# Performance work log

Hardware: AMD Instinct MI355X
Metric: run time of the kernel (lower is better)

Reference implementation:

```python
import jax, jax.numpy as jnp
import numpy as np

K_GRAD = 20        # num_nbrs for gradient operator
K_NORMAL = 10      # knn for normal/basis estimation
GRAD_REG = 1e-3    # grad_reg (lambda)
KERNEL_WIDTH = 1.0 # grad_kernel_width
EPS = 1e-8
N1, N2 = 8192, 8192
CHANNELS = [3, 64, 128, 256]


def knn_idx(pos, k):
    # brute-force kNN incl. self (loop=True, target_to_source)
    sq = jnp.sum(pos * pos, axis=1)
    d2 = sq[:, None] + sq[None, :] - 2.0 * (pos @ pos.T)
    _, idx = jax.lax.top_k(-d2, k)
    return idx  # [N, k]


def estimate_basis(pos, nbr, orientation):
    rel = pos[nbr] - pos[:, None, :]              # [N,k,3]
    cov = jnp.einsum('nki,nkj->nij', rel, rel)    # [N,3,3] local PCA
    _, vecs = jnp.linalg.eigh(cov)                # ascending eigenvalues
    normal, x_basis = vecs[:, :, 0], vecs[:, :, 2]
    sign = jnp.where(jnp.sum(normal * orientation, -1, keepdims=True) < 0.0, -1.0, 1.0)
    normal = normal * sign                        # orient along `orientation`
    y_basis = jnp.cross(normal, x_basis)
    return normal, x_basis, y_basis


def build_grad_div(pos, x_basis, y_basis, nbr):
    # regularized, Gaussian-weighted least-squares fit of a linear function per neighborhood
    rel = pos[nbr] - pos[:, None, :]              # [N,k,3]
    u = jnp.einsum('nkd,nd->nk', rel, x_basis)    # tangent coords
    v = jnp.einsum('nkd,nd->nk', rel, y_basis)
    dist = jnp.sqrt(jnp.sum(rel * rel, -1) + EPS)
    h = jnp.mean(dist, axis=1, keepdims=True)     # per-point bandwidth
    w = jnp.exp(-(dist * dist) / ((KERNEL_WIDTH * h) ** 2 + EPS))
    B = jnp.stack([jnp.ones_like(u), u, v], -1)   # [N,k,3] design matrix
    BtW = jnp.swapaxes(B, 1, 2) * w[:, None, :]   # [N,3,k]
    A = BtW @ B + GRAD_REG * jnp.eye(3, dtype=pos.dtype)
    C = jnp.linalg.solve(A, BtW)                  # [N,3,k] LS coefficients
    Gx, Gy = C[:, 1, :], C[:, 2, :]               # gradient stencils
    basis = jnp.stack([x_basis, y_basis], -1)     # [N,3,2]
    R = jnp.einsum('nda,nkdb->nkab', basis, basis[nbr])  # transport j->i, [N,k,2,2]
    return Gx, Gy, R


def grad_apply(Gx, Gy, nbr, f):
    fn = f[nbr]                                   # [N,k,C]
    return jnp.stack([jnp.einsum('nk,nkc->nc', Gx, fn),
                      jnp.einsum('nk,nkc->nc', Gy, fn)], 1)  # [N,2,C]


def div_apply(Gx, Gy, R, nbr, v):
    vt = jnp.einsum('nkab,nkbc->nkac', R, v[nbr])  # transported neighbor vectors
    return (jnp.einsum('nk,nkc->nc', Gx, vt[:, :, 0]) +
            jnp.einsum('nk,nkc->nc', Gy, vt[:, :, 1]))


def delta_conv(x, v, nbr, Gx, Gy, R, Ws, bs, Wv, bv, centralized):
    xn = x[nbr]
    if centralized:
        xn = xn - x[:, None, :]
    xmax = jnp.max(xn, axis=1)                    # max aggregation
    dv = div_apply(Gx, Gy, R, nbr, v)             # divergence
    Jv = jnp.stack([-v[:, 1], v[:, 0]], 1)        # 90-degree rotation
    cv = div_apply(Gx, Gy, R, nbr, Jv)            # curl = div(J v)
    x_out = jax.nn.relu(jnp.concatenate([xmax, dv, cv], -1) @ Ws + bs)
    if Wv is None:
        return x_out, v                            # last layer: scalar only
    gv = grad_apply(Gx, Gy, nbr, x_out)           # [N,2,Cout]
    vo = jnp.concatenate([v, gv], -1) @ Wv        # channel mix, no bias (equivariant)
    n = jnp.sqrt(jnp.sum(vo * vo, axis=1, keepdims=True) + EPS)
    vo = vo * (jax.nn.relu(n + bv) / (n + EPS))   # norm-gated vector nonlinearity
    return x_out, vo


def _forward(points, als_ppoints, params):
    pos = jnp.concatenate([points, als_ppoints], axis=0)  # [N,3]
    nbr = knn_idx(pos, K_GRAD)
    nbr_n = knn_idx(pos, K_NORMAL)
    _, xb, yb = estimate_basis(pos, nbr_n, orientation=pos)
    Gx, Gy, R = build_grad_div(pos, xb, yb, nbr)
    x = pos
    v = grad_apply(Gx, Gy, nbr, x)                # v = grad @ x
    out = []
    for i, (Ws, bs, Wv, bv) in enumerate(params):
        x, v = delta_conv(x, v, nbr, Gx, Gy, R, Ws, bs, Wv, bv, centralized=(i == 0))
        out.append(x)
    return tuple(out)


def setup_inputs():
    key = jax.random.key(0)
    ks = jax.random.split(key, 8)
    inp = {
        'points': jax.random.normal(ks[0], (N1, 3), jnp.float32),
        'als_ppoints': jax.random.normal(ks[1], (N2, 3), jnp.float32),
    }
    ki = 2
    for i in range(3):
        cin, cout = CHANNELS[i], CHANNELS[i + 1]
        inp[f'Ws{i}'] = jax.random.normal(ks[ki], (3 * cin, cout), jnp.float32) / np.sqrt(3.0 * cin)
        inp[f'bs{i}'] = jnp.zeros((cout,), jnp.float32)
        ki += 1
        if i < 2:
            inp[f'Wv{i}'] = jax.random.normal(ks[ki], (cin + cout, cout), jnp.float32) / np.sqrt(float(cin + cout))
            inp[f'bv{i}'] = jnp.zeros((cout,), jnp.float32)
            ki += 1
    return inp


def reference(points, als_ppoints, Ws0, bs0, Wv0, bv0, Ws1, bs1, Wv1, bv1, Ws2, bs2):
    params = [(Ws0, bs0, Wv0, bv0), (Ws1, bs1, Wv1, bv1), (Ws2, bs2, None, None)]
    return _forward(points, als_ppoints, params)
```

## Files before the change

kernel.cpp:

```cpp
#include <hip/hip_runtime.h>
#include <math.h>

#define NPTS 16384
#define KG 20
#define KN 10
#define KC 8
#define EPSF 1e-8f

#define GDIM 32
#define GL 4.75f
#define CW 0.296875f
#define GINV 3.3684210526f
#define RMAX 6

typedef __attribute__((ext_vector_type(8))) short short8v;
typedef __attribute__((ext_vector_type(4))) float floatx4;

__device__ __forceinline__ unsigned short f2bf(float v) {
  union { float f; unsigned u; } x;
  x.f = v;
  unsigned r = x.u + 0x7FFFu + ((x.u >> 16) & 1u);
  return (unsigned short)(r >> 16);
}

__device__ __forceinline__ float bf2f(unsigned short u) {
  union { unsigned u32; float f; } x;
  x.u32 = (unsigned)u << 16;
  return x.f;
}

#define KNN_INSERT(d2v, iv)                                                 \
  if ((d2v) < dist[KG - 1]) {                                               \
    dist[KG - 1] = (d2v); idx[KG - 1] = (iv);                               \
    _Pragma("unroll")                                                       \
    for (int s_ = KG - 1; s_ > 0; --s_) {                                   \
      if (dist[s_] < dist[s_ - 1]) {                                        \
        float td_ = dist[s_]; dist[s_] = dist[s_ - 1]; dist[s_ - 1] = td_;  \
        int ti_ = idx[s_]; idx[s_] = idx[s_ - 1]; idx[s_ - 1] = ti_;        \
      }                                                                     \
    }                                                                       \
  }

#define KNN_INSERT8(d2v, iv)                                                \
  if ((d2v) < dist[KC - 1]) {                                               \
    dist[KC - 1] = (d2v); idx[KC - 1] = (iv);                               \
    _Pragma("unroll")                                                       \
    for (int s_ = KC - 1; s_ > 0; --s_) {                                   \
      if (dist[s_] < dist[s_ - 1]) {                                        \
        float td_ = dist[s_]; dist[s_] = dist[s_ - 1]; dist[s_ - 1] = td_;  \
        int ti_ = idx[s_]; idx[s_] = idx[s_ - 1]; idx[s_ - 1] = ti_;        \
      }                                                                     \
    }                                                                       \
  }

__global__ __launch_bounds__(256) void posbin_kernel(const float* __restrict__ pts,
                                                     const float* __restrict__ als,
                                                     float4* __restrict__ pos4,
                                                     int* __restrict__ cell_count,
                                                     int* __restrict__ pt_cell) {
  int n = blockIdx.x * 256 + threadIdx.x;
  if (n >= NPTS) return;
  const float* src = (n < 8192) ? (pts + (size_t)n * 3) : (als + (size_t)(n - 8192) * 3);
  float x = src[0], y = src[1], z = src[2];
  pos4[n] = make_float4(x, y, z, 0.f);
  int cxi = (int)floorf((x + GL) * GINV); cxi = min(max(cxi, 0), GDIM - 1);
  int cyi = (int)floorf((y + GL) * GINV); cyi = min(max(cyi, 0), GDIM - 1);
  int czi = (int)floorf((z + GL) * GINV); czi = min(max(czi, 0), GDIM - 1);
  int c = (czi * GDIM + cyi) * GDIM + cxi;
  pt_cell[n] = c;
  atomicAdd(&cell_count[c], 1);
}

__global__ __launch_bounds__(256) void zero_kernel(int* __restrict__ cell_count,
                                                   int* __restrict__ fb_count) {
  int i = blockIdx.x * 256 + threadIdx.x;
  if (i < GDIM * GDIM * GDIM) cell_count[i] = 0;
  if (i == 0) *fb_count = 0;
}

__device__ __forceinline__ int cell_of(float x) {
  int c = (int)floorf((x + GL) * GINV);
  return min(max(c, 0), GDIM - 1);
}

__global__ __launch_bounds__(1024) void scan_kernel(const int* __restrict__ cell_count,
                                                    int* __restrict__ cell_start,
                                                    int* __restrict__ cell_cursor) {
  __shared__ int s[1024];
  int tid = threadIdx.x;
  int base = tid * 32;
  int local[32];
  int sum = 0;
#pragma unroll
  for (int i = 0; i < 32; ++i) { local[i] = cell_count[base + i]; sum += local[i]; }
  s[tid] = sum;
  __syncthreads();
  for (int off = 1; off < 1024; off <<= 1) {
    int v = (tid >= off) ? s[tid - off] : 0;
    __syncthreads();
    s[tid] += v;
    __syncthreads();
  }
  int run = s[tid] - sum;
#pragma unroll
  for (int i = 0; i < 32; ++i) {
    cell_start[base + i] = run;
    cell_cursor[base + i] = run;
    run += local[i];
  }
}

__global__ __launch_bounds__(256) void scatter_kernel(const float4* __restrict__ pos4,
                                                      const int* __restrict__ pt_cell,
                                                      int* __restrict__ cell_cursor,
                                                      float4* __restrict__ sorted4,
                                                      int* __restrict__ sortmap) {
  int i = blockIdx.x * 256 + threadIdx.x;
  if (i >= NPTS) return;
  int c = pt_cell[i];
  int dst = atomicAdd(&cell_cursor[c], 1);
  float4 p = pos4[i];
  p.w = __int_as_float(i);
  sorted4[dst] = p;
  sortmap[dst] = i;
}

__global__ __launch_bounds__(256) void knn_grid_kernel(const float4* __restrict__ sorted4,
                                                       const int* __restrict__ cell_start,
                                                       const int* __restrict__ cell_count,
                                                       int* __restrict__ nbr,
                                                       int* __restrict__ fb_list,
                                                       int* __restrict__ fb_count) {
  int lane = threadIdx.x & 63;
  int sub = lane >> 5;
  int sl = lane & 31;
  int qs = blockIdx.x * 8 + (threadIdx.x >> 6) * 2 + sub;
  if (qs >= NPTS) return;
  float4 p = sorted4[qs];
  int cx = cell_of(p.x), cy = cell_of(p.y), cz = cell_of(p.z);
  float dist[KC];
  int idx[KC];
#pragma unroll
  for (int i = 0; i < KC; ++i) { dist[i] = 3.4e38f; idx[i] = 0; }

  {
    int tot = 0;
    int x0 = max(cx - 1, 0), x1 = min(cx + 1, GDIM - 1);
    int zlo = max(cz - 1, 0), zhi = min(cz + 1, GDIM - 1);
    int ylo = max(cy - 1, 0), yhi = min(cy + 1, GDIM - 1);
    for (int z = zlo; z <= zhi; ++z) {
      for (int y = ylo; y <= yhi; ++y) {
        int c0 = (z * GDIM + y) * GDIM + x0;
        int c1 = (z * GDIM + y) * GDIM + x1;
        int beg = cell_start[c0];
        int end = cell_start[c1] + cell_count[c1];
        int off = (sl - tot) & 31;
        for (int j = beg + off; j < end; j += 32) {
          float4 sp = sorted4[j];
          float dx = sp.x - p.x, dy = sp.y - p.y, dz = sp.z - p.z;
          float d2 = dx * dx + dy * dy + dz * dz;
          KNN_INSERT8(d2, j);
        }
        tot += end - beg;
      }
    }
  }
  int done;
  {
    float b2 = CW * CW;
    int cnt = 0;
#pragma unroll
    for (int i = 0; i < KC; ++i) cnt += (dist[i] <= b2) ? 1 : 0;
#pragma unroll
    for (int s = 1; s < 32; s <<= 1) cnt += __shfl_xor(cnt, s, 64);
    done = (cnt >= KG) ? 1 : 0;
  }

  for (int r = 2; r <= RMAX && !done; ++r) {
    int side = 2 * r + 1;
    int nt = side * side;
    for (int t = sl; t < nt; t += 32) {
      int dz = t / side - r;
      int dy = t - (dz + r) * side - r;
      int z = cz + dz, y = cy + dy;
      if (z < 0 || z >= GDIM || y < 0 || y >= GDIM) continue;
      int rowbase = (z * GDIM + y) * GDIM;
      if (dz == -r || dz == r || dy == -r || dy == r) {
        int xa = max(cx - r, 0), xb = min(cx + r, GDIM - 1);
        int beg = cell_start[rowbase + xa];
        int end = cell_start[rowbase + xb] + cell_count[rowbase + xb];
        for (int j = beg; j < end; ++j) {
          float4 sp = sorted4[j];
          float ddx = sp.x - p.x, ddy = sp.y - p.y, ddz = sp.z - p.z;
          float d2 = ddx * ddx + ddy * ddy + ddz * ddz;
          KNN_INSERT8(d2, j);
        }
      } else {
        int x = cx - r;
        if (x >= 0) {
          int c = rowbase + x;
          int beg = cell_start[c], end = beg + cell_count[c];
          for (int j = beg; j < end; ++j) {
            float4 sp = sorted4[j];
            float ddx = sp.x - p.x, ddy = sp.y - p.y, ddz = sp.z - p.z;
            float d2 = ddx * ddx + ddy * ddy + ddz * ddz;
            KNN_INSERT8(d2, j);
          }
        }
        x = cx + r;
        if (x < GDIM) {
          int c = rowbase + x;
          int beg = cell_start[c], end = beg + cell_count[c];
          for (int j = beg; j < end; ++j) {
            float4 sp = sorted4[j];
            float ddx = sp.x - p.x, ddy = sp.y - p.y, ddz = sp.z - p.z;
            float d2 = ddx * ddx + ddy * ddy + ddz * ddz;
            KNN_INSERT8(d2, j);
          }
        }
      }
    }
    float b = CW * (float)r;
    float b2 = b * b;
    int cnt = 0;
#pragma unroll
    for (int i = 0; i < KC; ++i) cnt += (dist[i] <= b2) ? 1 : 0;
#pragma unroll
    for (int s = 1; s < 32; s <<= 1) cnt += __shfl_xor(cnt, s, 64);
    if (cnt >= KG) done = 1;
  }

  int popc = 0, ovf = 0;
  for (int round = 0; round < KG; ++round) {
    unsigned long long key = ((unsigned long long)__float_as_uint(dist[0]) << 14) |
                             (unsigned long long)(unsigned)idx[0];
    unsigned long long m = key;
#pragma unroll
    for (int s = 1; s < 32; s <<= 1) {
      unsigned long long o = __shfl_xor(m, s, 64);
      if (o < m) m = o;
    }
    if (key == m) {
      nbr[(size_t)qs * KG + round] = (int)(m & 0x3FFF);
#pragma unroll
      for (int s = 0; s < KC - 1; ++s) { dist[s] = dist[s + 1]; idx[s] = idx[s + 1]; }
      dist[KC - 1] = 3.4e38f;
      idx[KC - 1] = 0;
      if (++popc == KC) ovf = 1;
    }
  }
#pragma unroll
  for (int s = 1; s < 32; s <<= 1) ovf |= __shfl_xor(ovf, s, 64);
  if ((ovf || !done) && sl == 0) {
    int s = atomicAdd(fb_count, 1);
    fb_list[s] = qs;
  }
}

__global__ __launch_bounds__(256) void knn_fb_kernel(const float4* __restrict__ sorted4,
                                                     const int* __restrict__ fb_list,
                                                     const int* __restrict__ fb_count,
                                                     int* __restrict__ nbr) {
  __shared__ unsigned long long lists[256 * KG];
  __shared__ unsigned long long heads[256];
  __shared__ unsigned long long winner;
  int tid = threadIdx.x;
  int cnt = *fb_count;
  for (int qi = blockIdx.x; qi < cnt; qi += gridDim.x) {
    int t = fb_list[qi];
    float4 p = sorted4[t];
    float dist[KG];
    int idx[KG];
#pragma unroll
    for (int i = 0; i < KG; ++i) { dist[i] = 3.4e38f; idx[i] = 0; }
    int j0 = tid * 64;
    for (int j = j0; j < j0 + 64; ++j) {
      float4 c = sorted4[j];
      float dx = c.x - p.x, dy = c.y - p.y, dz = c.z - p.z;
      float d2 = dx * dx + dy * dy + dz * dz;
      KNN_INSERT(d2, j);
    }
#pragma unroll
    for (int i = 0; i < KG; ++i)
      lists[tid * KG + i] = ((unsigned long long)__float_as_uint(dist[i]) << 22) |
                            ((unsigned long long)(unsigned)idx[i] << 8) |
                            (unsigned long long)tid;
    int hp = 0;
    __syncthreads();
    for (int round = 0; round < KG; ++round) {
      heads[tid] = (hp < KG) ? lists[tid * KG + hp] : ~0ull;
      __syncthreads();
      if (tid < 64) {
        unsigned long long m = heads[tid];
        unsigned long long o = heads[tid + 64];  if (o < m) m = o;
        o = heads[tid + 128]; if (o < m) m = o;
        o = heads[tid + 192]; if (o < m) m = o;
#pragma unroll
        for (int s = 32; s > 0; s >>= 1) {
          unsigned long long x = __shfl_xor(m, s, 64);
          if (x < m) m = x;
        }
        if (tid == 0) winner = m;
      }
      __syncthreads();
      unsigned long long w = winner;
      if (tid == (int)(w & 0xFF)) hp++;
      if (tid == 0) nbr[(size_t)t * KG + round] = (int)((w >> 8) & 0x3FFF);
      __syncthreads();
    }
  }
}

__global__ __launch_bounds__(256) void basis_kernel(const float4* __restrict__ sorted4,
                                                    const int* __restrict__ nbr,
                                                    float4* __restrict__ xb4,
                                                    float4* __restrict__ yb4) {
  int n = blockIdx.x * 256 + threadIdx.x;
  if (n >= NPTS) return;
  float4 p = sorted4[n];
  double c00 = 0, c01 = 0, c02 = 0, c11 = 0, c12 = 0, c22 = 0;
  for (int k = 0; k < KN; ++k) {
    int m = nbr[(size_t)n * KG + k];
    float4 pm = sorted4[m];
    double dx = (double)pm.x - p.x, dy = (double)pm.y - p.y, dz = (double)pm.z - p.z;
    c00 += dx * dx; c01 += dx * dy; c02 += dx * dz;
    c11 += dy * dy; c12 += dy * dz; c22 += dz * dz;
  }
  double nx = 0, ny = 0, nz = 1;
  double p1 = c01 * c01 + c02 * c02 + c12 * c12;
  double qm = (c00 + c11 + c22) / 3.0;
  double g0 = c00 - qm, g1 = c11 - qm, g2 = c22 - qm;
  double p2 = g0 * g0 + g1 * g1 + g2 * g2 + 2.0 * p1;
  if (p2 > 1e-26) {
    double pp = sqrt(p2 / 6.0);
    double inv = 1.0 / pp;
    double b00 = g0 * inv, b11 = g1 * inv, b22 = g2 * inv;
    double b01 = c01 * inv, b02 = c02 * inv, b12 = c12 * inv;
    double detB = b00 * (b11 * b22 - b12 * b12) - b01 * (b01 * b22 - b12 * b02) +
                  b02 * (b01 * b12 - b11 * b02);
    double r = 0.5 * detB;
    r = fmin(1.0, fmax(-1.0, r));
    double phi = acos(r) / 3.0;
    double e1 = qm + 2.0 * pp * cos(phi);
    double e3 = qm + 2.0 * pp * cos(phi + 2.0943951023931953);
    double e2 = 3.0 * qm - e1 - e3;
    double a00 = c00 - e1, a11 = c11 - e1, a22 = c22 - e1;
    double f00 = c00 - e2, f11 = c11 - e2, f22 = c22 - e2;
    double u0 = a00 * f00 + c01 * c01 + c02 * c02;
    double u1 = c01 * f00 + a11 * c01 + c12 * c02;
    double u2 = c02 * f00 + c12 * c01 + a22 * c02;
    double v0 = a00 * c01 + c01 * f11 + c02 * c12;
    double v1 = c01 * c01 + a11 * f11 + c12 * c12;
    double v2 = c02 * c01 + c12 * f11 + a22 * c12;
    double w0 = a00 * c02 + c01 * c12 + c02 * f22;
    double w1 = c01 * c02 + a11 * c12 + c12 * f22;
    double w2 = c02 * c02 + c12 * c12 + a22 * f22;
    double nu = u0 * u0 + u1 * u1 + u2 * u2;
    double nv = v0 * v0 + v1 * v1 + v2 * v2;
    double nw = w0 * w0 + w1 * w1 + w2 * w2;
    double bx = u0, by = u1, bz = u2, bn = nu;
    if (nv > bn) { bx = v0; by = v1; bz = v2; bn = nv; }
    if (nw > bn) { bx = w0; by = w1; bz = w2; bn = nw; }
    if (bn > 1e-40) {
      double s = 1.0 / sqrt(bn);
      nx = bx * s; ny = by * s; nz = bz * s;
    }
  }
  double dotp = nx * p.x + ny * p.y + nz * p.z;
  if (dotp < 0.0) { nx = -nx; ny = -ny; nz = -nz; }
  double ax = fabs(nx), ay = fabs(ny), az = fabs(nz);
  double ex = 0, ey = 0, ez = 0;
  if (ax <= ay && ax <= az) ex = 1;
  else if (ay <= az) ey = 1;
  else ez = 1;
  double tx = ny * ez - nz * ey, ty = nz * ex - nx * ez, tz = nx * ey - ny * ex;
  double tn = 1.0 / sqrt(tx * tx + ty * ty + tz * tz);
  tx *= tn; ty *= tn; tz *= tn;
  double ux = ny * tz - nz * ty, uy = nz * tx - nx * tz, uz = nx * ty - ny * tx;
  xb4[n] = make_float4((float)tx, (float)ty, (float)tz, 0.f);
  yb4[n] = make_float4((float)ux, (float)uy, (float)uz, 0.f);
}

__global__ __launch_bounds__(256) void graddiv_kernel(const float4* __restrict__ sorted4,
                                                      const int* __restrict__ nbr,
                                                      const float4* __restrict__ xb4,
                                                      const float4* __restrict__ yb4,
                                                      float* __restrict__ Gx,
                                                      float* __restrict__ Gy,
                                                      float2* __restrict__ C2,
                                                      float* __restrict__ v0) {
  int n = blockIdx.x * 256 + threadIdx.x;
  if (n >= NPTS) return;
  float4 p = sorted4[n], xb = xb4[n], yb = yb4[n];
  float u[KG], vv[KG], w[KG];
  int mm[KG];
  float hsum = 0.f;
#pragma unroll
  for (int k = 0; k < KG; ++k) {
    int m = nbr[(size_t)n * KG + k];
    mm[k] = m;
    float4 pm = sorted4[m];
    float rx = pm.x - p.x, ry = pm.y - p.y, rz = pm.z - p.z;
    u[k] = rx * xb.x + ry * xb.y + rz * xb.z;
    vv[k] = rx * yb.x + ry * yb.y + rz * yb.z;
    float dd = sqrtf(rx * rx + ry * ry + rz * rz + EPSF);
    w[k] = dd; hsum += dd;
  }
  float h = hsum * (1.f / KG);
  float invden = 1.f / (h * h + EPSF);
  double A00 = 0, A01 = 0, A02 = 0, A11 = 0, A12 = 0, A22 = 0;
#pragma unroll
  for (int k = 0; k < KG; ++k) {
    float wk = expf(-(w[k] * w[k]) * invden);
    w[k] = wk;
    A00 += wk; A01 += (double)wk * u[k]; A02 += (double)wk * vv[k];
    A11 += (double)wk * u[k] * u[k]; A12 += (double)wk * u[k] * vv[k];
    A22 += (double)wk * vv[k] * vv[k];
  }
  A00 += 0.001; A11 += 0.001; A22 += 0.001;
  double det = A00 * (A11 * A22 - A12 * A12) - A01 * (A01 * A22 - A12 * A02) +
               A02 * (A01 * A12 - A11 * A02);
  double idet = 1.0 / det;
  float i10 = (float)((A02 * A12 - A01 * A22) * idet);
  float i11 = (float)((A00 * A22 - A02 * A02) * idet);
  float i12 = (float)((A01 * A02 - A00 * A12) * idet);
  float i20 = (float)((A01 * A12 - A02 * A11) * idet);
  float i21 = i12;
  float i22 = (float)((A00 * A11 - A01 * A01) * idet);
  float a0x = 0, a0y = 0, a0z = 0, a1x = 0, a1y = 0, a1z = 0;
#pragma unroll
  for (int k = 0; k < KG; ++k) {
    float gx = w[k] * (i10 + i11 * u[k] + i12 * vv[k]);
    float gy = w[k] * (i20 + i21 * u[k] + i22 * vv[k]);
    Gx[(size_t)n * KG + k] = gx;
    Gy[(size_t)n * KG + k] = gy;
    int m = mm[k];
    float4 pm = sorted4[m];
    a0x += gx * pm.x; a0y += gx * pm.y; a0z += gx * pm.z;
    a1x += gy * pm.x; a1y += gy * pm.y; a1z += gy * pm.z;
    float4 xm = xb4[m], ym = yb4[m];
    float g3x = gx * xb.x + gy * yb.x;
    float g3y = gx * xb.y + gy * yb.y;
    float g3z = gx * xb.z + gy * yb.z;
    float ca = g3x * xm.x + g3y * xm.y + g3z * xm.z;
    float cb = g3x * ym.x + g3y * ym.y + g3z * ym.z;
    C2[(size_t)n * KG + k] = make_float2(ca, cb);
  }
  v0[((size_t)n * 2 + 0) * 3 + 0] = a0x;
  v0[((size_t)n * 2 + 0) * 3 + 1] = a0y;
  v0[((size_t)n * 2 + 0) * 3 + 2] = a0z;
  v0[((size_t)n * 2 + 1) * 3 + 0] = a1x;
  v0[((size_t)n * 2 + 1) * 3 + 1] = a1y;
  v0[((size_t)n * 2 + 1) * 3 + 2] = a1z;
}

template <int CENTRAL>
__global__ __launch_bounds__(256) void feat16_kernel(const float* __restrict__ x, int ldx,
                                                     int cin,
                                                     const float* __restrict__ v,
                                                     const int* __restrict__ nbr,
                                                     const float2* __restrict__ C2,
                                                     unsigned short* __restrict__ feat, int Kp) {
  int per = Kp - 2 * cin;
  int gid = blockIdx.x * 256 + threadIdx.x;
  if (gid >= NPTS * per) return;
  int n = gid / per;
  int c = gid - n * per;
  size_t fb = (size_t)n * Kp;
  if (c >= cin) {
    feat[fb + 3 * cin + (c - cin)] = 0;
    return;
  }
  float xc = x[(size_t)n * ldx + c];
  float xmax = -3.4e38f, dv = 0.f, cv = 0.f;
  for (int k = 0; k < KG; ++k) {
    int m = nbr[(size_t)n * KG + k];
    float2 cc = C2[(size_t)n * KG + k];
    float xm = x[(size_t)m * ldx + c];
    xmax = fmaxf(xmax, CENTRAL ? (xm - xc) : xm);
    float va = v[((size_t)m * 2 + 0) * cin + c];
    float vb = v[((size_t)m * 2 + 1) * cin + c];
    dv += cc.x * va + cc.y * vb;
    cv += cc.y * va - cc.x * vb;
  }
  feat[fb + c] = f2bf(xmax);
  feat[fb + cin + c] = f2bf(dv);
  feat[fb + 2 * cin + c] = f2bf(cv);
}

__global__ __launch_bounds__(256) void feat16v8_kernel(const unsigned short* __restrict__ x,
                                                       int cin,
                                                       const unsigned short* __restrict__ v,
                                                       const int* __restrict__ nbr,
                                                       const float2* __restrict__ C2,
                                                       unsigned short* __restrict__ feat) {
  int per = cin >> 3;
  int gid = blockIdx.x * 256 + threadIdx.x;
  if (gid >= NPTS * per) return;
  int n = gid / per;
  int c8 = (gid - n * per) << 3;
  float xmax[8], dv[8], cv[8];
#pragma unroll
  for (int i = 0; i < 8; ++i) { xmax[i] = -3.4e38f; dv[i] = 0.f; cv[i] = 0.f; }
  const int* nrow = nbr + (size_t)n * KG;
  const float2* crow = C2 + (size_t)n * KG;
#pragma unroll 4
  for (int k = 0; k < KG; ++k) {
    int m = nrow[k];
    float2 cc = crow[k];
    short8v xm = *reinterpret_cast<const short8v*>(x + (size_t)m * cin + c8);
    short8v va = *reinterpret_cast<const short8v*>(v + ((size_t)m * 2 + 0) * cin + c8);
    short8v vb = *reinterpret_cast<const short8v*>(v + ((size_t)m * 2 + 1) * cin + c8);
#pragma unroll
    for (int i = 0; i < 8; ++i) {
      float xf = bf2f((unsigned short)xm[i]);
      float af = bf2f((unsigned short)va[i]);
      float bf = bf2f((unsigned short)vb[i]);
      xmax[i] = fmaxf(xmax[i], xf);
      dv[i] += cc.x * af + cc.y * bf;
      cv[i] += cc.y * af - cc.x * bf;
    }
  }
  size_t fb = (size_t)n * (3 * cin);
  short8v o0, o1, o2;
#pragma unroll
  for (int i = 0; i < 8; ++i) {
    o0[i] = (short)f2bf(xmax[i]);
    o1[i] = (short)f2bf(dv[i]);
    o2[i] = (short)f2bf(cv[i]);
  }
  *reinterpret_cast<short8v*>(&feat[fb + c8]) = o0;
  *reinterpret_cast<short8v*>(&feat[fb + cin + c8]) = o1;
  *reinterpret_cast<short8v*>(&feat[fb + 2 * cin + c8]) = o2;
}

__global__ __launch_bounds__(256) void vin16_kernel(const float* __restrict__ v, int cin,
                                                    const unsigned short* __restrict__ xout,
                                                    int cout,
                                                    const int* __restrict__ nbr,
                                                    const float* __restrict__ Gx,
                                                    const float* __restrict__ Gy,
                                                    unsigned short* __restrict__ vinb, int Kp,
                                                    int total) {
  int gid = blockIdx.x * 256 + threadIdx.x;
  if (gid >= total) return;
  int n = gid / Kp;
  int c = gid - n * Kp;
  int K = cin + cout;
  unsigned short o0, o1;
  if (c < cin) {
    o0 = f2bf(v[((size_t)n * 2 + 0) * cin + c]);
    o1 = f2bf(v[((size_t)n * 2 + 1) * cin + c]);
  } else if (c < K) {
    int cc = c - cin;
    float a0 = 0.f, a1 = 0.f;
    for (int k = 0; k < KG; ++k) {
      int m = nbr[(size_t)n * KG + k];
      float f = bf2f(xout[(size_t)m * cout + cc]);
      a0 += Gx[(size_t)n * KG + k] * f;
      a1 += Gy[(size_t)n * KG + k] * f;
    }
    o0 = f2bf(a0);
    o1 = f2bf(a1);
  } else {
    o0 = 0; o1 = 0;
  }
  vinb[((size_t)n * 2 + 0) * Kp + c] = o0;
  vinb[((size_t)n * 2 + 1) * Kp + c] = o1;
}

__global__ __launch_bounds__(256) void vin16v8_kernel(const unsigned short* __restrict__ v,
                                                      int cin,
                                                      const unsigned short* __restrict__ xout,
                                                      int cout,
                                                      const int* __restrict__ nbr,
                                                      const float* __restrict__ Gx,
                                                      const float* __restrict__ Gy,
                                                      unsigned short* __restrict__ vinb,
                                                      int Kp) {
  int per = Kp >> 3;
  int gid = blockIdx.x * 256 + threadIdx.x;
  if (gid >= NPTS * per) return;
  int n = gid / per;
  int c8 = (gid - n * per) << 3;
  short8v o0, o1;
  if (c8 < cin) {
    o0 = *reinterpret_cast<const short8v*>(v + ((size_t)n * 2 + 0) * cin + c8);
    o1 = *reinterpret_cast<const short8v*>(v + ((size_t)n * 2 + 1) * cin + c8);
  } else {
    int cc8 = c8 - cin;
    float a0[8], a1[8];
#pragma unroll
    for (int i = 0; i < 8; ++i) { a0[i] = 0.f; a1[i] = 0.f; }
    const int* nrow = nbr + (size_t)n * KG;
    const float* gxr = Gx + (size_t)n * KG;
    const float* gyr = Gy + (size_t)n * KG;
#pragma unroll 4
    for (int k = 0; k < KG; ++k) {
      int m = nrow[k];
      float gx = gxr[k], gy = gyr[k];
      short8v f = *reinterpret_cast<const short8v*>(xout + (size_t)m * cout + cc8);
#pragma unroll
      for (int i = 0; i < 8; ++i) {
        float ff = bf2f((unsigned short)f[i]);
        a0[i] += gx * ff;
        a1[i] += gy * ff;
      }
    }
#pragma unroll
    for (int i = 0; i < 8; ++i) {
      o0[i] = (short)f2bf(a0[i]);
      o1[i] = (short)f2bf(a1[i]);
    }
  }
  *reinterpret_cast<short8v*>(&vinb[((size_t)n * 2 + 0) * Kp + c8]) = o0;
  *reinterpret_cast<short8v*>(&vinb[((size_t)n * 2 + 1) * Kp + c8]) = o1;
}

__device__ __forceinline__ void wprep_one(const float* W, unsigned short* Wt, int K, int Kp,
                                          int N, int i) {
  int n = i / Kp, k = i - n * Kp;
  Wt[i] = (k < K) ? f2bf(W[(size_t)k * N + n]) : (unsigned short)0;
}

__global__ __launch_bounds__(256) void wprep_all_kernel(const float* __restrict__ Ws0,
                                                        const float* __restrict__ Wv0,
                                                        const float* __restrict__ Ws1,
                                                        const float* __restrict__ Wv1,
                                                        const float* __restrict__ Ws2,
                                                        unsigned short* __restrict__ Wt_s0,
                                                        unsigned short* __restrict__ Wt_v0,
                                                        unsigned short* __restrict__ Wt_s1,
                                                        unsigned short* __restrict__ Wt_v1,
                                                        unsigned short* __restrict__ Wt_s2) {
  int gid = blockIdx.x * 256 + threadIdx.x;
  if (gid < 2048) wprep_one(Ws0, Wt_s0, 9, 32, 64, gid);
  else if (gid < 8192) wprep_one(Wv0, Wt_v0, 67, 96, 64, gid - 2048);
  else if (gid < 32768) wprep_one(Ws1, Wt_s1, 192, 192, 128, gid - 8192);
  else if (gid < 57344) wprep_one(Wv1, Wt_v1, 192, 192, 128, gid - 32768);
  else if (gid < 155648) wprep_one(Ws2, Wt_s2, 384, 384, 256, gid - 57344);
}

template <int MODE>
__global__ __launch_bounds__(256) void gemm16_kernel(const unsigned short* __restrict__ A,
                                                     const unsigned short* __restrict__ Bt,
                                                     const float* __restrict__ bias,
                                                     float* __restrict__ Cf,
                                                     unsigned short* __restrict__ Cb,
                                                     const int* __restrict__ rowmap,
                                                     int Kp, int Ncol) {
  int lane = threadIdx.x & 63;
  int wave = threadIdx.x >> 6;
  int rowBase = blockIdx.y * 64 + wave * 16;
  int colBase = blockIdx.x * 64;
  int lr = lane & 15;
  int kg = (lane >> 4) * 8;
  floatx4 acc0 = {0.f, 0.f, 0.f, 0.f};
  floatx4 acc1 = acc0, acc2 = acc0, acc3 = acc0;
  const unsigned short* arow = A + (size_t)(rowBase + lr) * Kp + kg;
  const unsigned short* b0p = Bt + (size_t)(colBase + lr) * Kp + kg;
  for (int k0 = 0; k0 < Kp; k0 += 32) {
    short8v a = *reinterpret_cast<const short8v*>(arow + k0);
    short8v b0 = *reinterpret_cast<const short8v*>(b0p + k0);
    short8v b1 = *reinterpret_cast<const short8v*>(b0p + (size_t)16 * Kp + k0);
    short8v b2 = *reinterpret_cast<const short8v*>(b0p + (size_t)32 * Kp + k0);
    short8v b3 = *reinterpret_cast<const short8v*>(b0p + (size_t)48 * Kp + k0);
    acc0 = __builtin_amdgcn_mfma_f32_16x16x32_bf16(a, b0, acc0, 0, 0, 0);
    acc1 = __builtin_amdgcn_mfma_f32_16x16x32_bf16(a, b1, acc1, 0, 0, 0);
    acc2 = __builtin_amdgcn_mfma_f32_16x16x32_bf16(a, b2, acc2, 0, 0, 0);
    acc3 = __builtin_amdgcn_mfma_f32_16x16x32_bf16(a, b3, acc3, 0, 0, 0);
  }
  int rsub = (lane >> 4) * 4;
  floatx4 accs[4] = {acc0, acc1, acc2, acc3};
  int orow[4];
  if (MODE == 0) {
#pragma unroll
    for (int r = 0; r < 4; ++r) orow[r] = rowmap[rowBase + rsub + r];
  }
#pragma unroll
  for (int nb = 0; nb < 4; ++nb) {
    int col = colBase + nb * 16 + lr;
    float bb = bias[col];
    if (MODE == 0) {
#pragma unroll
      for (int r = 0; r < 4; ++r) {
        int row = rowBase + rsub + r;
        float val = fmaxf(accs[nb][r] + bb, 0.f);
        Cf[(size_t)orow[r] * Ncol + col] = val;
        if (Cb) Cb[(size_t)row * Ncol + col] = f2bf(val);
      }
    } else {
#pragma unroll
      for (int pr = 0; pr < 2; ++pr) {
        float a0 = accs[nb][2 * pr], a1 = accs[nb][2 * pr + 1];
        float nrm = sqrtf(a0 * a0 + a1 * a1 + EPSF);
        float s = fmaxf(nrm + bb, 0.f) / (nrm + EPSF);
        int row = rowBase + rsub + 2 * pr;
        Cb[(size_t)row * Ncol + col] = f2bf(a0 * s);
        Cb[(size_t)(row + 1) * Ncol + col] = f2bf(a1 * s);
      }
    }
  }
}

extern "C" void kernel_launch(void* const* d_in, const int* in_sizes, int n_in,
                              void* d_out, int out_size, void* d_ws, size_t ws_size,
                              hipStream_t stream) {
  const float* pts = (const float*)d_in[0];
  const float* als = (const float*)d_in[1];
  const float* Ws0 = (const float*)d_in[2];
  const float* bs0 = (const float*)d_in[3];
  const float* Wv0 = (const float*)d_in[4];
  const float* bv0 = (const float*)d_in[5];
  const float* Ws1 = (const float*)d_in[6];
  const float* bs1 = (const float*)d_in[7];
  const float* Wv1 = (const float*)d_in[8];
  const float* bv1 = (const float*)d_in[9];
  const float* Ws2 = (const float*)d_in[10];
  const float* bs2 = (const float*)d_in[11];

  char* ws = (char*)d_ws;
  float4* pos4 = (float4*)(ws + 0);
  int* nbr = (int*)(ws + 262144);
  float4* xb4 = (float4*)(ws + 1572864);
  float4* yb4 = (float4*)(ws + 1835008);
  float* Gx = (float*)(ws + 2097152);
  float* Gy = (float*)(ws + 3407872);
  float2* C2 = (float2*)(ws + 4718592);
  float* v0f = (float*)(ws + 7340032);
  unsigned short* vb_a = (unsigned short*)(ws + 8388608);
  unsigned short* vb_b = (unsigned short*)(ws + 17825792);
  unsigned short* xb0m = (unsigned short*)(ws + 23068672);
  unsigned short* xb1m = (unsigned short*)(ws + 26214400);
  unsigned short* stg = (unsigned short*)(ws + 31457280);
  char* wtb = ws + 45088768;
  unsigned short* Wt_s0 = (unsigned short*)(wtb + 0);
  unsigned short* Wt_v0 = (unsigned short*)(wtb + 4096);
  unsigned short* Wt_s1 = (unsigned short*)(wtb + 16384);
  unsigned short* Wt_v1 = (unsigned short*)(wtb + 65536);
  unsigned short* Wt_s2 = (unsigned short*)(wtb + 114688);

  char* gws = ws + 46137344;
  int* cell_count = (int*)(gws + 0);
  int* cell_start = (int*)(gws + 131072);
  int* cell_cursor = (int*)(gws + 262144);
  int* pt_cell = (int*)(gws + 393216);
  int* fb_list = (int*)(gws + 458752);
  int* fb_count = (int*)(gws + 524288);
  float4* sorted4 = (float4*)(gws + 528384);
  int* sortmap = (int*)(gws + 790528);

  float* out0 = (float*)d_out;
  float* out1 = out0 + (size_t)NPTS * 64;
  float* out2 = out1 + (size_t)NPTS * 128;

  zero_kernel<<<(GDIM * GDIM * GDIM + 255) / 256, 256, 0, stream>>>(cell_count, fb_count);
  posbin_kernel<<<64, 256, 0, stream>>>(pts, als, pos4, cell_count, pt_cell);
  scan_kernel<<<1, 1024, 0, stream>>>(cell_count, cell_start, cell_cursor);
  scatter_kernel<<<64, 256, 0, stream>>>(pos4, pt_cell, cell_cursor, sorted4, sortmap);
  knn_grid_kernel<<<NPTS / 8, 256, 0, stream>>>(sorted4, cell_start, cell_count, nbr, fb_list,
                                                fb_count);
  knn_fb_kernel<<<128, 256, 0, stream>>>(sorted4, fb_list, fb_count, nbr);

  basis_kernel<<<64, 256, 0, stream>>>(sorted4, nbr, xb4, yb4);
  graddiv_kernel<<<64, 256, 0, stream>>>(sorted4, nbr, xb4, yb4, Gx, Gy, C2, v0f);

  wprep_all_kernel<<<608, 256, 0, stream>>>(Ws0, Wv0, Ws1, Wv1, Ws2, Wt_s0, Wt_v0, Wt_s1,
                                            Wt_v1, Wt_s2);

  feat16_kernel<1><<<(NPTS * 26 + 255) / 256, 256, 0, stream>>>((const float*)sorted4, 4, 3,
                                                                v0f, nbr, C2, stg, 32);
  gemm16_kernel<0><<<dim3(1, 256), 256, 0, stream>>>(stg, Wt_s0, bs0, out0, xb0m, sortmap, 32,
                                                     64);
  vin16_kernel<<<(NPTS * 96 + 255) / 256, 256, 0, stream>>>(v0f, 3, xb0m, 64, nbr, Gx, Gy, stg,
                                                            96, NPTS * 96);
  gemm16_kernel<1><<<dim3(1, 512), 256, 0, stream>>>(stg, Wt_v0, bv0, nullptr, vb_b, nullptr,
                                                     96, 64);

  feat16v8_kernel<<<NPTS * 8 / 256, 256, 0, stream>>>(xb0m, 64, vb_b, nbr, C2, stg);
  gemm16_kernel<0><<<dim3(2, 256), 256, 0, stream>>>(stg, Wt_s1, bs1, out1, xb1m, sortmap, 192,
                                                     128);
  vin16v8_kernel<<<NPTS * 24 / 256, 256, 0, stream>>>(vb_b, 64, xb1m, 128, nbr, Gx, Gy, stg,
                                                      192);
  gemm16_kernel<1><<<dim3(2, 512), 256, 0, stream>>>(stg, Wt_v1, bv1, nullptr, vb_a, nullptr,
                                                     192, 128);

  feat16v8_kernel<<<NPTS * 16 / 256, 256, 0, stream>>>(xb1m, 128, vb_a, nbr, C2, stg);
  gemm16_kernel<0><<<dim3(4, 256), 256, 0, stream>>>(stg, Wt_s2, bs2, out2, nullptr, sortmap,
                                                     384, 256);
}
```

Measured before the change: 299.1 us.

## Use fp32 for basis and LS solve, shrink kNN candidate list, faster index math

Converts the per-point PCA eigen-solve in basis_kernel and the 3x3 least-squares accumulation and inverse in graddiv_kernel from double to float, using fast intrinsics (__cosf, __expf). It also shrinks the per-lane kNN candidate list from 8 to 6 and replaces an integer division in the shell traversal with a float reciprocal multiply. The aim is to avoid slow fp64 math and reduce the insertion-sort cost in the kNN search. The risks are reduced accuracy in near-degenerate eigenvectors and solves, and possibly wrong neighbors if 6 candidates per lane across 32 lanes is too few in dense regions.

```diff
diff --git a/kernel.cpp b/kernel.cpp
--- a/kernel.cpp
+++ b/kernel.cpp
@@ -4,7 +4,7 @@
 #define NPTS 16384
 #define KG 20
 #define KN 10
-#define KC 8
+#define KC 6
 #define EPSF 1e-8f
 
 #define GDIM 32
@@ -41,7 +41,7 @@
     }                                                                       \
   }
 
-#define KNN_INSERT8(d2v, iv)                                                \
+#define KNN_INSERTC(d2v, iv)                                                \
   if ((d2v) < dist[KC - 1]) {                                               \
     dist[KC - 1] = (d2v); idx[KC - 1] = (iv);                               \
     _Pragma("unroll")                                                       \
@@ -159,7 +159,7 @@
           float4 sp = sorted4[j];
           float dx = sp.x - p.x, dy = sp.y - p.y, dz = sp.z - p.z;
           float d2 = dx * dx + dy * dy + dz * dz;
-          KNN_INSERT8(d2, j);
+          KNN_INSERTC(d2, j);
         }
         tot += end - beg;
       }
@@ -179,9 +179,11 @@
   for (int r = 2; r <= RMAX && !done; ++r) {
     int side = 2 * r + 1;
     int nt = side * side;
+    float rcp = 1.0f / (float)side;
     for (int t = sl; t < nt; t += 32) {
-      int dz = t / side - r;
-      int dy = t - (dz + r) * side - r;
+      int qz = (int)(((float)t + 0.5f) * rcp);
+      int dz = qz - r;
+      int dy = t - qz * side - r;
       int z = cz + dz, y = cy + dy;
       if (z < 0 || z >= GDIM || y < 0 || y >= GDIM) continue;
       int rowbase = (z * GDIM + y) * GDIM;
@@ -193,7 +195,7 @@
           float4 sp = sorted4[j];
           float ddx = sp.x - p.x, ddy = sp.y - p.y, ddz = sp.z - p.z;
           float d2 = ddx * ddx + ddy * ddy + ddz * ddz;
-          KNN_INSERT8(d2, j);
+          KNN_INSERTC(d2, j);
         }
       } else {
         int x = cx - r;
@@ -204,7 +206,7 @@
             float4 sp = sorted4[j];
             float ddx = sp.x - p.x, ddy = sp.y - p.y, ddz = sp.z - p.z;
             float d2 = ddx * ddx + ddy * ddy + ddz * ddz;
-            KNN_INSERT8(d2, j);
+            KNN_INSERTC(d2, j);
           }
         }
         x = cx + r;
@@ -215,7 +217,7 @@
             float4 sp = sorted4[j];
             float ddx = sp.x - p.x, ddy = sp.y - p.y, ddz = sp.z - p.z;
             float d2 = ddx * ddx + ddy * ddy + ddz * ddz;
-            KNN_INSERT8(d2, j);
+            KNN_INSERTC(d2, j);
           }
         }
       }
@@ -318,67 +320,67 @@
   int n = blockIdx.x * 256 + threadIdx.x;
   if (n >= NPTS) return;
   float4 p = sorted4[n];
-  double c00 = 0, c01 = 0, c02 = 0, c11 = 0, c12 = 0, c22 = 0;
+  float c00 = 0, c01 = 0, c02 = 0, c11 = 0, c12 = 0, c22 = 0;
   for (int k = 0; k < KN; ++k) {
     int m = nbr[(size_t)n * KG + k];
     float4 pm = sorted4[m];
-    double dx = (double)pm.x - p.x, dy = (double)pm.y - p.y, dz = (double)pm.z - p.z;
+    float dx = pm.x - p.x, dy = pm.y - p.y, dz = pm.z - p.z;
     c00 += dx * dx; c01 += dx * dy; c02 += dx * dz;
     c11 += dy * dy; c12 += dy * dz; c22 += dz * dz;
   }
-  double nx = 0, ny = 0, nz = 1;
-  double p1 = c01 * c01 + c02 * c02 + c12 * c12;
-  double qm = (c00 + c11 + c22) / 3.0;
-  double g0 = c00 - qm, g1 = c11 - qm, g2 = c22 - qm;
-  double p2 = g0 * g0 + g1 * g1 + g2 * g2 + 2.0 * p1;
-  if (p2 > 1e-26) {
-    double pp = sqrt(p2 / 6.0);
-    double inv = 1.0 / pp;
-    double b00 = g0 * inv, b11 = g1 * inv, b22 = g2 * inv;
-    double b01 = c01 * inv, b02 = c02 * inv, b12 = c12 * inv;
-    double detB = b00 * (b11 * b22 - b12 * b12) - b01 * (b01 * b22 - b12 * b02) +
-                  b02 * (b01 * b12 - b11 * b02);
-    double r = 0.5 * detB;
-    r = fmin(1.0, fmax(-1.0, r));
-    double phi = acos(r) / 3.0;
-    double e1 = qm + 2.0 * pp * cos(phi);
-    double e3 = qm + 2.0 * pp * cos(phi + 2.0943951023931953);
-    double e2 = 3.0 * qm - e1 - e3;
-    double a00 = c00 - e1, a11 = c11 - e1, a22 = c22 - e1;
-    double f00 = c00 - e2, f11 = c11 - e2, f22 = c22 - e2;
-    double u0 = a00 * f00 + c01 * c01 + c02 * c02;
-    double u1 = c01 * f00 + a11 * c01 + c12 * c02;
-    double u2 = c02 * f00 + c12 * c01 + a22 * c02;
-    double v0 = a00 * c01 + c01 * f11 + c02 * c12;
-    double v1 = c01 * c01 + a11 * f11 + c12 * c12;
-    double v2 = c02 * c01 + c12 * f11 + a22 * c12;
-    double w0 = a00 * c02 + c01 * c12 + c02 * f22;
-    double w1 = c01 * c02 + a11 * c12 + c12 * f22;
-    double w2 = c02 * c02 + c12 * c12 + a22 * f22;
-    double nu = u0 * u0 + u1 * u1 + u2 * u2;
-    double nv = v0 * v0 + v1 * v1 + v2 * v2;
-    double nw = w0 * w0 + w1 * w1 + w2 * w2;
-    double bx = u0, by = u1, bz = u2, bn = nu;
+  float nx = 0.f, ny = 0.f, nz = 1.f;
+  float p1 = c01 * c01 + c02 * c02 + c12 * c12;
+  float qm = (c00 + c11 + c22) * (1.f / 3.f);
+  float g0 = c00 - qm, g1 = c11 - qm, g2 = c22 - qm;
+  float p2 = g0 * g0 + g1 * g1 + g2 * g2 + 2.f * p1;
+  if (p2 > 1e-16f) {
+    float pp = sqrtf(p2 * (1.f / 6.f));
+    float inv = 1.f / pp;
+    float b00 = g0 * inv, b11 = g1 * inv, b22 = g2 * inv;
+    float b01 = c01 * inv, b02 = c02 * inv, b12 = c12 * inv;
+    float detB = b00 * (b11 * b22 - b12 * b12) - b01 * (b01 * b22 - b12 * b02) +
+                 b02 * (b01 * b12 - b11 * b02);
+    float r = 0.5f * detB;
+    r = fminf(1.f, fmaxf(-1.f, r));
+    float phi = acosf(r) * (1.f / 3.f);
+    float e1 = qm + 2.f * pp * __cosf(phi);
+    float e3 = qm + 2.f * pp * __cosf(phi + 2.0943951023931953f);
+    float e2 = 3.f * qm - e1 - e3;
+    float a00 = c00 - e1, a11 = c11 - e1, a22 = c22 - e1;
+    float f00 = c00 - e2, f11 = c11 - e2, f22 = c22 - e2;
+    float u0 = a00 * f00 + c01 * c01 + c02 * c02;
+    float u1 = c01 * f00 + a11 * c01 + c12 * c02;
+    float u2 = c02 * f00 + c12 * c01 + a22 * c02;
+    float v0 = a00 * c01 + c01 * f11 + c02 * c12;
+    float v1 = c01 * c01 + a11 * f11 + c12 * c12;
+    float v2 = c02 * c01 + c12 * f11 + a22 * c12;
+    float w0 = a00 * c02 + c01 * c12 + c02 * f22;
+    float w1 = c01 * c02 + a11 * c12 + c12 * f22;
+    float w2 = c02 * c02 + c12 * c12 + a22 * f22;
+    float nu = u0 * u0 + u1 * u1 + u2 * u2;
+    float nv = v0 * v0 + v1 * v1 + v2 * v2;
+    float nw = w0 * w0 + w1 * w1 + w2 * w2;
+    float bx = u0, by = u1, bz = u2, bn = nu;
     if (nv > bn) { bx = v0; by = v1; bz = v2; bn = nv; }
     if (nw > bn) { bx = w0; by = w1; bz = w2; bn = nw; }
-    if (bn > 1e-40) {
-      double s = 1.0 / sqrt(bn);
+    if (bn > 1e-30f) {
+      float s = 1.f / sqrtf(bn);
       nx = bx * s; ny = by * s; nz = bz * s;
     }
   }
-  double dotp = nx * p.x + ny * p.y + nz * p.z;
-  if (dotp < 0.0) { nx = -nx; ny = -ny; nz = -nz; }
-  double ax = fabs(nx), ay = fabs(ny), az = fabs(nz);
-  double ex = 0, ey = 0, ez = 0;
-  if (ax <= ay && ax <= az) ex = 1;
-  else if (ay <= az) ey = 1;
-  else ez = 1;
-  double tx = ny * ez - nz * ey, ty = nz * ex - nx * ez, tz = nx * ey - ny * ex;
-  double tn = 1.0 / sqrt(tx * tx + ty * ty + tz * tz);
+  float dotp = nx * p.x + ny * p.y + nz * p.z;
+  if (dotp < 0.f) { nx = -nx; ny = -ny; nz = -nz; }
+  float ax = fabsf(nx), ay = fabsf(ny), az = fabsf(nz);
+  float ex = 0.f, ey = 0.f, ez = 0.f;
+  if (ax <= ay && ax <= az) ex = 1.f;
+  else if (ay <= az) ey = 1.f;
+  else ez = 1.f;
+  float tx = ny * ez - nz * ey, ty = nz * ex - nx * ez, tz = nx * ey - ny * ex;
+  float tn = 1.f / sqrtf(tx * tx + ty * ty + tz * tz);
   tx *= tn; ty *= tn; tz *= tn;
-  double ux = ny * tz - nz * ty, uy = nz * tx - nx * tz, uz = nx * ty - ny * tx;
-  xb4[n] = make_float4((float)tx, (float)ty, (float)tz, 0.f);
-  yb4[n] = make_float4((float)ux, (float)uy, (float)uz, 0.f);
+  float ux = ny * tz - nz * ty, uy = nz * tx - nx * tz, uz = nx * ty - ny * tx;
+  xb4[n] = make_float4(tx, ty, tz, 0.f);
+  yb4[n] = make_float4(ux, uy, uz, 0.f);
 }
 
 __global__ __launch_bounds__(256) void graddiv_kernel(const float4* __restrict__ sorted4,
@@ -408,25 +410,25 @@
   }
   float h = hsum * (1.f / KG);
   float invden = 1.f / (h * h + EPSF);
-  double A00 = 0, A01 = 0, A02 = 0, A11 = 0, A12 = 0, A22 = 0;
+  float A00 = 0, A01 = 0, A02 = 0, A11 = 0, A12 = 0, A22 = 0;
 #pragma unroll
   for (int k = 0; k < KG; ++k) {
-    float wk = expf(-(w[k] * w[k]) * invden);
+    float wk = __expf(-(w[k] * w[k]) * invden);
     w[k] = wk;
-    A00 += wk; A01 += (double)wk * u[k]; A02 += (double)wk * vv[k];
-    A11 += (double)wk * u[k] * u[k]; A12 += (double)wk * u[k] * vv[k];
-    A22 += (double)wk * vv[k] * vv[k];
-  }
-  A00 += 0.001; A11 += 0.001; A22 += 0.001;
-  double det = A00 * (A11 * A22 - A12 * A12) - A01 * (A01 * A22 - A12 * A02) +
-               A02 * (A01 * A12 - A11 * A02);
-  double idet = 1.0 / det;
-  float i10 = (float)((A02 * A12 - A01 * A22) * idet);
-  float i11 = (float)((A00 * A22 - A02 * A02) * idet);
-  float i12 = (float)((A01 * A02 - A00 * A12) * idet);
-  float i20 = (float)((A01 * A12 - A02 * A11) * idet);
+    A00 += wk; A01 += wk * u[k]; A02 += wk * vv[k];
+    A11 += wk * u[k] * u[k]; A12 += wk * u[k] * vv[k];
+    A22 += wk * vv[k] * vv[k];
+  }
+  A00 += 0.001f; A11 += 0.001f; A22 += 0.001f;
+  float det = A00 * (A11 * A22 - A12 * A12) - A01 * (A01 * A22 - A12 * A02) +
+              A02 * (A01 * A12 - A11 * A02);
+  float idet = 1.f / det;
+  float i10 = (A02 * A12 - A01 * A22) * idet;
+  float i11 = (A00 * A22 - A02 * A02) * idet;
+  float i12 = (A01 * A02 - A00 * A12) * idet;
+  float i20 = (A01 * A12 - A02 * A11) * idet;
   float i21 = i12;
-  float i22 = (float)((A00 * A11 - A01 * A01) * idet);
+  float i22 = (A00 * A11 - A01 * A01) * idet;
   float a0x = 0, a0y = 0, a0z = 0, a1x = 0, a1y = 0, a1z = 0;
 #pragma unroll
   for (int k = 0; k < KG; ++k) {
```

Measured after the change: 290.8 us. -2.8%, faster.
